# Kernel optimization log

Measured on AMD Instinct MI355X. Metric: run time of the kernel, lower is better.

## Reference

```python
import jax, jax.numpy as jnp
import numpy as np

N = 100000       # nodes
E = 1600000      # edges (before self-loops)
D_IN = 128       # input feature dim
HID = 16         # hidden channels per head
HEADS = 4
D_OUT = 32       # output communities
NEG_SLOPE = 0.2  # PyG GATConv default leaky_relu slope


def setup_inputs() -> dict:
    key = jax.random.key(0)
    ks = jax.random.split(key, 10)
    s = 0.1
    x = jax.random.normal(ks[0], (N, D_IN), jnp.float32)
    edge_index = jax.random.randint(ks[1], (2, E), 0, N, dtype=jnp.int64)
    W1 = jax.random.normal(ks[2], (D_IN, HEADS * HID), jnp.float32) * s
    a_src1 = jax.random.normal(ks[3], (HEADS, HID), jnp.float32) * s
    a_dst1 = jax.random.normal(ks[4], (HEADS, HID), jnp.float32) * s
    b1 = jnp.zeros((HEADS * HID,), jnp.float32)
    W2 = jax.random.normal(ks[5], (HEADS * HID, D_OUT), jnp.float32) * s
    a_src2 = jax.random.normal(ks[6], (1, D_OUT), jnp.float32) * s
    a_dst2 = jax.random.normal(ks[7], (1, D_OUT), jnp.float32) * s
    b2 = jnp.zeros((D_OUT,), jnp.float32)
    return {"x": x, "edge_index": edge_index, "W1": W1, "a_src1": a_src1,
            "a_dst1": a_dst1, "b1": b1, "W2": W2, "a_src2": a_src2,
            "a_dst2": a_dst2, "b2": b2}


def _segment_softmax(logits, seg, n):
    # softmax over edges grouped by destination node (per head)
    m = jax.ops.segment_max(logits, seg, num_segments=n)
    m = jnp.where(jnp.isfinite(m), m, 0.0)  # guard empty segments
    e = jnp.exp(logits - m[seg])
    z = jax.ops.segment_sum(e, seg, num_segments=n)
    return e / (z[seg] + 1e-16)


def _gat_conv(x, src, dst, W, a_src, a_dst, bias, heads, out_c, concat):
    n = x.shape[0]
    h = (x @ W).reshape(n, heads, out_c)                 # [N,H,C]
    al_s = jnp.einsum('nhc,hc->nh', h, a_src)            # [N,H]
    al_d = jnp.einsum('nhc,hc->nh', h, a_dst)            # [N,H]
    logits = jax.nn.leaky_relu(al_s[src] + al_d[dst], NEG_SLOPE)  # [E,H]
    alpha = _segment_softmax(logits, dst, n)             # [E,H]
    msg = h[src] * alpha[..., None]                      # [E,H,C]
    out = jax.ops.segment_sum(msg, dst, num_segments=n)  # [N,H,C]
    out = out.reshape(n, heads * out_c) if concat else out.mean(axis=1)
    return out + bias


def reference(x, edge_index, W1, a_src1, a_dst1, b1, W2, a_src2, a_dst2, b2):
    loops = jnp.arange(N, dtype=edge_index.dtype)
    src = jnp.concatenate([edge_index[0], loops])
    dst = jnp.concatenate([edge_index[1], loops])
    h = _gat_conv(x, src, dst, W1, a_src1, a_dst1, b1, HEADS, HID, True)
    h = jax.nn.elu(h)
    return _gat_conv(h, src, dst, W2, a_src2, a_dst2, b2, 1, D_OUT, False)
```

## Files before the change

kernel.cpp:

```cpp
#include <hip/hip_runtime.h>
#include <hip/hip_fp16.h>
#include <math.h>

#define NN 100000
#define EE 1600000
#define DIN 128
#define C1 64
#define C2 32
#define NEG 0.2f

#define NB 1024
#define BSH 7
#define EPB 4096
#define NGEMM 1563
#define NCHIST 391

static __device__ __forceinline__ float leaky(float x) { return fmaxf(x, NEG * x); }

__global__ __launch_bounds__(256, 2) void k_gemm1_chist(
    const float* __restrict__ x, const float* __restrict__ W1,
    const float* __restrict__ a_s, const float* __restrict__ a_d,
    __half* __restrict__ h1h, float* __restrict__ als, float* __restrict__ ald,
    const int* __restrict__ ei, int* __restrict__ bhist) {
    __shared__ float xs[64 * 128];
    __shared__ float wsh[128 * 64];
    int t = threadIdx.x;
    if (blockIdx.x >= NGEMM) {
        int* h = (int*)xs;
        for (int i = t; i < NB; i += 256) h[i] = 0;
        __syncthreads();
        const int4* d4p = (const int4*)(ei + EE);
        int i40 = (blockIdx.x - NGEMM) * (EPB / 4);
#pragma unroll
        for (int j = 0; j < 4; j++) {
            int idx = i40 + t + 256 * j;
            if (idx < EE / 4) {
                int4 d4 = d4p[idx];
                atomicAdd(&h[d4.x >> BSH], 1);
                atomicAdd(&h[d4.y >> BSH], 1);
                atomicAdd(&h[d4.z >> BSH], 1);
                atomicAdd(&h[d4.w >> BSH], 1);
            }
        }
        __syncthreads();
        for (int i = t; i < NB; i += 256) {
            int c = h[i];
            if (c) atomicAdd(&bhist[i], c);
        }
        return;
    }
    int base = blockIdx.x * 64;
    for (int i = t; i < 2048; i += 256) ((float4*)wsh)[i] = ((const float4*)W1)[i];
    int maxn = NN - base;
    if (maxn > 64) maxn = 64;
    for (int i = t; i < 2048; i += 256) {
        int flat = i * 4;
        int n = flat >> 7;
        if (n < maxn) *(float4*)&xs[flat] = *(const float4*)&x[(size_t)(base + n) * 128 + (flat & 127)];
    }
    __syncthreads();
    int w = t >> 6, c = t & 63;
    int nb = w * 16;
    float acc[16];
#pragma unroll
    for (int j = 0; j < 16; j++) acc[j] = 0.f;
    for (int k = 0; k < 128; k += 4) {
        float w0 = wsh[k * 64 + c], w1 = wsh[(k + 1) * 64 + c];
        float w2 = wsh[(k + 2) * 64 + c], w3 = wsh[(k + 3) * 64 + c];
#pragma unroll
        for (int j = 0; j < 16; j++) {
            float4 xv = *(float4*)&xs[(nb + j) * 128 + k];
            acc[j] = fmaf(xv.x, w0, acc[j]);
            acc[j] = fmaf(xv.y, w1, acc[j]);
            acc[j] = fmaf(xv.z, w2, acc[j]);
            acc[j] = fmaf(xv.w, w3, acc[j]);
        }
    }
    float s_a = a_s[c], d_a = a_d[c];
    int hd = c >> 4;
#pragma unroll
    for (int j = 0; j < 16; j++) {
        int n = base + nb + j;
        float v = acc[j];
        float vs = v * s_a, vd = v * d_a;
#pragma unroll
        for (int off = 1; off < 16; off <<= 1) {
            vs += __shfl_xor(vs, off, 64);
            vd += __shfl_xor(vd, off, 64);
        }
        if (n < NN) {
            h1h[(size_t)n * 64 + c] = __float2half(v);
            if ((c & 15) == 0) {
                als[n * 4 + hd] = vs;
                ald[n * 4 + hd] = vd;
            }
        }
    }
}


__global__ __launch_bounds__(256) void k_bscan(const int* __restrict__ bhist,
                                               int* __restrict__ gbase, int* __restrict__ gcur) {
    __shared__ int s[256];
    int t = threadIdx.x;
    int base = t * 4;
    int v[4];
    int run = 0;
#pragma unroll
    for (int j = 0; j < 4; j++) {
        v[j] = run;
        run += bhist[base + j];
    }
    int val = run;
    s[t] = val;
    __syncthreads();
    for (int off = 1; off < 256; off <<= 1) {
        int add = (t >= off) ? s[t - off] : 0;
        __syncthreads();
        val += add;
        s[t] = val;
        __syncthreads();
    }
    int texcl = val - run;
#pragma unroll
    for (int j = 0; j < 4; j++) {
        gbase[base + j] = texcl + v[j];
        gcur[base + j] = texcl + v[j];
    }
}

__global__ __launch_bounds__(256) void k_bin(const int* __restrict__ ei, int* __restrict__ gcur,
                                             int* __restrict__ binned) {
    __shared__ int h[NB];
    __shared__ int base[NB];
    int t = threadIdx.x;
    for (int i = t; i < NB; i += 256) h[i] = 0;
    __syncthreads();
    const int4* s4p = (const int4*)ei;
    const int4* d4p = (const int4*)(ei + EE);
    int i40 = blockIdx.x * (EPB / 4);
    int4 s4[4], d4[4];
    bool val[4];
#pragma unroll
    for (int j = 0; j < 4; j++) {
        int idx = i40 + t + 256 * j;
        val[j] = idx < EE / 4;
        if (val[j]) {
            s4[j] = s4p[idx];
            d4[j] = d4p[idx];
            atomicAdd(&h[d4[j].x >> BSH], 1);
            atomicAdd(&h[d4[j].y >> BSH], 1);
            atomicAdd(&h[d4[j].z >> BSH], 1);
            atomicAdd(&h[d4[j].w >> BSH], 1);
        }
    }
    __syncthreads();
    for (int i = t; i < NB; i += 256) {
        int c = h[i];
        if (c) base[i] = atomicAdd(&gcur[i], c);
        h[i] = 0;
    }
    __syncthreads();
#pragma unroll
    for (int j = 0; j < 4; j++) {
        if (val[j]) {
            int ss[4] = {s4[j].x, s4[j].y, s4[j].z, s4[j].w};
            int dd[4] = {d4[j].x, d4[j].y, d4[j].z, d4[j].w};
#pragma unroll
            for (int q = 0; q < 4; q++) {
                int b = dd[q] >> BSH;
                int r = atomicAdd(&h[b], 1);
                binned[base[b] + r] = (ss[q] << 7) | (dd[q] & 127);
            }
        }
    }
}

__global__ __launch_bounds__(256) void k_bsort(const int* __restrict__ binned,
                                               const int* __restrict__ gbase,
                                               const int* __restrict__ bhist,
                                               int* __restrict__ rs, int* __restrict__ deg,
                                               int* __restrict__ csr) {
    __shared__ int h[128], cur[128], sc[128];
    int b = blockIdx.x, t = threadIdx.x;
    if (t < 128) h[t] = 0;
    __syncthreads();
    int gb = gbase[b], cnt = bhist[b];
    for (int i = t; i < cnt; i += 256) atomicAdd(&h[binned[gb + i] & 127], 1);
    __syncthreads();
    if (t < 128) sc[t] = h[t];
    __syncthreads();
    for (int off = 1; off < 128; off <<= 1) {
        int add = 0;
        if (t < 128 && t >= off) add = sc[t - off];
        __syncthreads();
        if (t < 128) sc[t] += add;
        __syncthreads();
    }
    if (t < 128) {
        int node = b * 128 + t;
        int excl = sc[t] - h[t];
        if (node < NN) {
            rs[node] = gb + excl;
            deg[node] = h[t];
        }
        cur[t] = excl;
    }
    __syncthreads();
    for (int i = t; i < cnt; i += 256) {
        int e = binned[gb + i];
        int r = atomicAdd(&cur[e & 127], 1);
        csr[gb + r] = e >> 7;
    }
}

__global__ __launch_bounds__(256, 4) void k_edge1(
    const int* __restrict__ csr, const int* __restrict__ rs, const int* __restrict__ deg,
    const __half* __restrict__ h1h, const float* __restrict__ als, const float* __restrict__ ald,
    const float* __restrict__ b1, const float* __restrict__ W2,
    const float* __restrict__ as2, const float* __restrict__ ad2,
    __half* __restrict__ h2h, float* __restrict__ als2, float* __restrict__ ald2) {
    __shared__ float wsh[64 * 32];
    __shared__ float xld[4][64];
    __shared__ float2 epl[4][4][65];
    int t = threadIdx.x;
    for (int i = t; i < 512; i += 256) ((float4*)wsh)[i] = ((const float4*)W2)[i];
    int w = t >> 6, lane = t & 63;
    int n = blockIdx.x * 4 + w;
    float4 ad4 = *(const float4*)&ald[n * 4];
    float4 an4 = *(const float4*)&als[n * 4];
    float ls0 = leaky(an4.x + ad4.x), ls1 = leaky(an4.y + ad4.y);
    float ls2 = leaky(an4.z + ad4.z), ls3 = leaky(an4.w + ad4.w);
    const __half2* h1p = (const __half2*)h1h;
    int cc = lane & 31, eh = lane >> 5;
    int hd2 = cc >> 3;
    float z = 0.f, acc0 = 0.f, acc1 = 0.f;
    if (eh == 0) {
        float2 fs = __half22float2(h1p[n * 32 + cc]);
        z = 1.f;
        acc0 = fs.x;
        acc1 = fs.y;
    }
    int s0 = rs[n], d = deg[n];
    for (int i0 = 0; i0 < d; i0 += 64) {
        int e = i0 + lane;
        int src = 0;
        float4 a4 = make_float4(-1e30f, -1e30f, -1e30f, -1e30f);
        if (e < d) {
            src = csr[s0 + e];
            a4 = *(const float4*)&als[src * 4];
        }
        float fsrc = __int_as_float(src);
        epl[w][0][lane] = make_float2(fsrc, __expf(leaky(a4.x + ad4.x) - ls0));
        epl[w][1][lane] = make_float2(fsrc, __expf(leaky(a4.y + ad4.y) - ls1));
        epl[w][2][lane] = make_float2(fsrc, __expf(leaky(a4.z + ad4.z) - ls2));
        epl[w][3][lane] = make_float2(fsrc, __expf(leaky(a4.w + ad4.w) - ls3));
        int cnt = d - i0;
        if (cnt > 64) cnt = 64;
        int i = eh;
        for (; i + 14 < cnt; i += 16) {
            float2 q0 = epl[w][hd2][i], q1 = epl[w][hd2][i + 2];
            float2 q2 = epl[w][hd2][i + 4], q3 = epl[w][hd2][i + 6];
            float2 q4 = epl[w][hd2][i + 8], q5 = epl[w][hd2][i + 10];
            float2 q6 = epl[w][hd2][i + 12], q7 = epl[w][hd2][i + 14];
            float2 f0 = __half22float2(h1p[__float_as_int(q0.x) * 32 + cc]);
            float2 f1 = __half22float2(h1p[__float_as_int(q1.x) * 32 + cc]);
            float2 f2 = __half22float2(h1p[__float_as_int(q2.x) * 32 + cc]);
            float2 f3 = __half22float2(h1p[__float_as_int(q3.x) * 32 + cc]);
            float2 f4 = __half22float2(h1p[__float_as_int(q4.x) * 32 + cc]);
            float2 f5 = __half22float2(h1p[__float_as_int(q5.x) * 32 + cc]);
            float2 f6 = __half22float2(h1p[__float_as_int(q6.x) * 32 + cc]);
            float2 f7 = __half22float2(h1p[__float_as_int(q7.x) * 32 + cc]);
            z += ((q0.y + q1.y) + (q2.y + q3.y)) + ((q4.y + q5.y) + (q6.y + q7.y));
            acc0 = fmaf(q0.y, f0.x, acc0); acc1 = fmaf(q0.y, f0.y, acc1);
            acc0 = fmaf(q1.y, f1.x, acc0); acc1 = fmaf(q1.y, f1.y, acc1);
            acc0 = fmaf(q2.y, f2.x, acc0); acc1 = fmaf(q2.y, f2.y, acc1);
            acc0 = fmaf(q3.y, f3.x, acc0); acc1 = fmaf(q3.y, f3.y, acc1);
            acc0 = fmaf(q4.y, f4.x, acc0); acc1 = fmaf(q4.y, f4.y, acc1);
            acc0 = fmaf(q5.y, f5.x, acc0); acc1 = fmaf(q5.y, f5.y, acc1);
            acc0 = fmaf(q6.y, f6.x, acc0); acc1 = fmaf(q6.y, f6.y, acc1);
            acc0 = fmaf(q7.y, f7.x, acc0); acc1 = fmaf(q7.y, f7.y, acc1);
        }
        for (; i + 6 < cnt; i += 8) {
            float2 q0 = epl[w][hd2][i], q1 = epl[w][hd2][i + 2];
            float2 q2 = epl[w][hd2][i + 4], q3 = epl[w][hd2][i + 6];
            float2 f0 = __half22float2(h1p[__float_as_int(q0.x) * 32 + cc]);
            float2 f1 = __half22float2(h1p[__float_as_int(q1.x) * 32 + cc]);
            float2 f2 = __half22float2(h1p[__float_as_int(q2.x) * 32 + cc]);
            float2 f3 = __half22float2(h1p[__float_as_int(q3.x) * 32 + cc]);
            z += (q0.y + q1.y) + (q2.y + q3.y);
            acc0 = fmaf(q0.y, f0.x, acc0); acc1 = fmaf(q0.y, f0.y, acc1);
            acc0 = fmaf(q1.y, f1.x, acc0); acc1 = fmaf(q1.y, f1.y, acc1);
            acc0 = fmaf(q2.y, f2.x, acc0); acc1 = fmaf(q2.y, f2.y, acc1);
            acc0 = fmaf(q3.y, f3.x, acc0); acc1 = fmaf(q3.y, f3.y, acc1);
        }
        for (; i < cnt; i += 2) {
            float2 q = epl[w][hd2][i];
            float2 f = __half22float2(h1p[__float_as_int(q.x) * 32 + cc]);
            z += q.y;
            acc0 = fmaf(q.y, f.x, acc0);
            acc1 = fmaf(q.y, f.y, acc1);
        }
    }
    acc0 += __shfl_xor(acc0, 32, 64);
    acc1 += __shfl_xor(acc1, 32, 64);
    z += __shfl_xor(z, 32, 64);
    float zi = __frcp_rn(z + 1e-16f);
    float o0 = acc0 * zi + b1[2 * cc];
    float o1 = acc1 * zi + b1[2 * cc + 1];
    float xv0 = o0 > 0.f ? o0 : __expf(o0) - 1.f;
    float xv1 = o1 > 0.f ? o1 : __expf(o1) - 1.f;
    if (eh == 0) {
        xld[w][2 * cc] = xv0;
        xld[w][2 * cc + 1] = xv1;
    }
    __syncthreads();

    int hi = lane >> 5, c2 = lane & 31;
    float accn = 0.f;
#pragma unroll
    for (int k = 0; k < 32; k++) {
        float xk = xld[w][hi * 32 + k];
        accn = fmaf(xk, wsh[(hi * 32 + k) * 32 + c2], accn);
    }
    accn += __shfl_xor(accn, 32, 64);
    float vs = accn * as2[c2], vd = accn * ad2[c2];
#pragma unroll
    for (int off = 1; off < 32; off <<= 1) {
        vs += __shfl_xor(vs, off, 64);
        vd += __shfl_xor(vd, off, 64);
    }
    if (lane < 32) h2h[(size_t)n * 32 + lane] = __float2half(accn);
    if (lane == 0) {
        als2[n] = vs;
        ald2[n] = vd;
    }
}

__global__ __launch_bounds__(256, 4) void k_edge2(
    const int* __restrict__ csr, const int* __restrict__ rs, const int* __restrict__ deg,
    const __half* __restrict__ h2h, const float* __restrict__ als, const float* __restrict__ ald,
    const float* __restrict__ b2, float* __restrict__ out) {
    __shared__ float2 pst[4][64];
    int t = threadIdx.x;
    int w = t >> 6, lane = t & 63;
    int n = blockIdx.x * 4 + w;
    int cc = lane & 15, eq = lane >> 4;
    float ad = ald[n];
    float lself = leaky(als[n] + ad);
    const __half2* h2p = (const __half2*)h2h;
    float z = 0.f, acc0 = 0.f, acc1 = 0.f;
    if (eq == 0) {
        float2 fs = __half22float2(h2p[n * 16 + cc]);
        z = 1.f;
        acc0 = fs.x;
        acc1 = fs.y;
    }
    int s0 = rs[n], d = deg[n];
    for (int i0 = 0; i0 < d; i0 += 64) {
        int e = i0 + lane;
        int src = 0;
        float av = -1e30f;
        if (e < d) {
            src = csr[s0 + e];
            av = als[src];
        }
        float p = __expf(leaky(av + ad) - lself);
        pst[w][lane] = make_float2(__int_as_float(src), p);
        int cnt = d - i0;
        if (cnt > 64) cnt = 64;
        int i = eq;
        for (; i + 12 < cnt; i += 16) {
            float2 qA = pst[w][i], qB = pst[w][i + 4], qC = pst[w][i + 8], qD = pst[w][i + 12];
            int sA = __float_as_int(qA.x), sB = __float_as_int(qB.x);
            int sC = __float_as_int(qC.x), sD = __float_as_int(qD.x);
            float2 fA = __half22float2(h2p[sA * 16 + cc]);
            float2 fB = __half22float2(h2p[sB * 16 + cc]);
            float2 fC = __half22float2(h2p[sC * 16 + cc]);
            float2 fD = __half22float2(h2p[sD * 16 + cc]);
            z += (qA.y + qB.y) + (qC.y + qD.y);
            acc0 = fmaf(qA.y, fA.x, acc0); acc1 = fmaf(qA.y, fA.y, acc1);
            acc0 = fmaf(qB.y, fB.x, acc0); acc1 = fmaf(qB.y, fB.y, acc1);
            acc0 = fmaf(qC.y, fC.x, acc0); acc1 = fmaf(qC.y, fC.y, acc1);
            acc0 = fmaf(qD.y, fD.x, acc0); acc1 = fmaf(qD.y, fD.y, acc1);
        }
        for (; i < cnt; i += 4) {
            float2 q = pst[w][i];
            int sA = __float_as_int(q.x);
            float pA = q.y;
            float2 f = __half22float2(h2p[sA * 16 + cc]);
            z += pA;
            acc0 = fmaf(pA, f.x, acc0);
            acc1 = fmaf(pA, f.y, acc1);
        }
    }
    acc0 += __shfl_xor(acc0, 16, 64);
    acc0 += __shfl_xor(acc0, 32, 64);
    acc1 += __shfl_xor(acc1, 16, 64);
    acc1 += __shfl_xor(acc1, 32, 64);
    z += __shfl_xor(z, 16, 64);
    z += __shfl_xor(z, 32, 64);
    if (eq == 0) {
        float zi = __frcp_rn(z + 1e-16f);
        float o0 = acc0 * zi + b2[2 * cc];
        float o1 = acc1 * zi + b2[2 * cc + 1];
        *(float2*)&out[(size_t)n * 32 + 2 * cc] = make_float2(o0, o1);
    }
}

extern "C" void kernel_launch(void* const* d_in, const int* in_sizes, int n_in,
                              void* d_out, int out_size, void* d_ws, size_t ws_size,
                              hipStream_t stream) {
    const float* x = (const float*)d_in[0];
    const int* ei = (const int*)d_in[1];
    const float* W1 = (const float*)d_in[2];
    const float* as1 = (const float*)d_in[3];
    const float* ad1 = (const float*)d_in[4];
    const float* b1 = (const float*)d_in[5];
    const float* W2 = (const float*)d_in[6];
    const float* as2 = (const float*)d_in[7];
    const float* ad2 = (const float*)d_in[8];
    const float* b2 = (const float*)d_in[9];
    float* out = (float*)d_out;

    char* p = (char*)d_ws;
    auto alloc = [&](size_t bytes) -> char* {
        char* r = p;
        p += (bytes + 255) & ~(size_t)255;
        return r;
    };
    int* csr = (int*)alloc((size_t)EE * 4);
    int* rs = (int*)alloc((size_t)NN * 4);
    int* deg = (int*)alloc((size_t)NN * 4);
    int* bhist = (int*)alloc(NB * 4);
    int* gbase = (int*)alloc(NB * 4);
    int* gcur = (int*)alloc(NB * 4);
    __half* h1h = (__half*)alloc((size_t)NN * C1 * 2);
    float* als1 = (float*)alloc((size_t)NN * 4 * 4);
    float* ald1 = (float*)alloc((size_t)NN * 4 * 4);
    char* regionX = alloc((size_t)NN * C2 * 2 + (size_t)NN * 8 + 512);
    int* binned = (int*)regionX;
    __half* h2h = (__half*)regionX;
    float* als2 = (float*)(regionX + (size_t)NN * C2 * 2);
    float* ald2 = (float*)(regionX + (size_t)NN * C2 * 2 + (size_t)NN * 4);
    (void)ws_size;

    hipMemsetAsync(bhist, 0, NB * 4, stream);

    k_gemm1_chist<<<NGEMM + NCHIST, 256, 0, stream>>>(x, W1, as1, ad1, h1h, als1, ald1,
                                                      ei, bhist);
    k_bscan<<<1, 256, 0, stream>>>(bhist, gbase, gcur);
    k_bin<<<NCHIST, 256, 0, stream>>>(ei, gcur, binned);
    k_bsort<<<(NN + 127) / 128, 256, 0, stream>>>(binned, gbase, bhist, rs, deg, csr);

    k_edge1<<<NN / 4, 256, 0, stream>>>(csr, rs, deg, h1h, als1, ald1, b1, W2, as2, ad2,
                                        h2h, als2, ald2);
    k_edge2<<<NN / 4, 256, 0, stream>>>(csr, rs, deg, h2h, als2, ald2, b2, out);
}
```

Measured before the change: 332.3 us.

## Map more nodes per wavefront in edge kernels and pack row start with degree

k_edge1 now assigns one node per half-wavefront (32 lanes) instead of one per wavefront, and k_edge2 one node per quarter-wavefront (16 lanes). This removes the cross-lane reductions and the idle lanes that low-degree nodes (average degree 16) left in the old edge-split scheme. Source indices are pre-shifted into byte offsets to simplify gather addressing. The row start and degree arrays are merged into one int2 array. W2 is stored transposed in shared memory so the second GEMM can use float4 reads, and the grids shrink to match. Nodes with large degree now run more serial iterations per group, which risks more load imbalance within a wavefront.

Result: faster. 293.0 us (-11.8%).

```diff
diff --git a/kernel.cpp b/kernel.cpp
--- a/kernel.cpp
+++ b/kernel.cpp
@@ -179,7 +179,7 @@
 __global__ __launch_bounds__(256) void k_bsort(const int* __restrict__ binned,
                                                const int* __restrict__ gbase,
                                                const int* __restrict__ bhist,
-                                               int* __restrict__ rs, int* __restrict__ deg,
+                                               int2* __restrict__ rsdeg,
                                                int* __restrict__ csr) {
     __shared__ int h[128], cur[128], sc[128];
     int b = blockIdx.x, t = threadIdx.x;
@@ -200,10 +200,7 @@
     if (t < 128) {
         int node = b * 128 + t;
         int excl = sc[t] - h[t];
-        if (node < NN) {
-            rs[node] = gb + excl;
-            deg[node] = h[t];
-        }
+        if (node < NN) rsdeg[node] = make_int2(gb + excl, h[t]);
         cur[t] = excl;
     }
     __syncthreads();
@@ -215,62 +212,58 @@
 }
 
 __global__ __launch_bounds__(256, 4) void k_edge1(
-    const int* __restrict__ csr, const int* __restrict__ rs, const int* __restrict__ deg,
+    const int* __restrict__ csr, const int2* __restrict__ rsdeg,
     const __half* __restrict__ h1h, const float* __restrict__ als, const float* __restrict__ ald,
     const float* __restrict__ b1, const float* __restrict__ W2,
     const float* __restrict__ as2, const float* __restrict__ ad2,
     __half* __restrict__ h2h, float* __restrict__ als2, float* __restrict__ ald2) {
-    __shared__ float wsh[64 * 32];
-    __shared__ float xld[4][64];
-    __shared__ float2 epl[4][4][65];
+    __shared__ float wsh[32][68];
+    __shared__ float xld[4][2][64];
+    __shared__ float2 epl[4][2][4][33];
     int t = threadIdx.x;
-    for (int i = t; i < 512; i += 256) ((float4*)wsh)[i] = ((const float4*)W2)[i];
-    int w = t >> 6, lane = t & 63;
-    int n = blockIdx.x * 4 + w;
+    for (int i = t; i < 2048; i += 256) wsh[i & 31][i >> 5] = W2[i];
+    int w = t >> 6, lane = t & 63, half = lane >> 5, ln = lane & 31;
+    int n = blockIdx.x * 8 + w * 2 + half;
     float4 ad4 = *(const float4*)&ald[n * 4];
     float4 an4 = *(const float4*)&als[n * 4];
     float ls0 = leaky(an4.x + ad4.x), ls1 = leaky(an4.y + ad4.y);
     float ls2 = leaky(an4.z + ad4.z), ls3 = leaky(an4.w + ad4.w);
     const __half2* h1p = (const __half2*)h1h;
-    int cc = lane & 31, eh = lane >> 5;
-    int hd2 = cc >> 3;
-    float z = 0.f, acc0 = 0.f, acc1 = 0.f;
-    if (eh == 0) {
-        float2 fs = __half22float2(h1p[n * 32 + cc]);
-        z = 1.f;
-        acc0 = fs.x;
-        acc1 = fs.y;
-    }
-    int s0 = rs[n], d = deg[n];
-    for (int i0 = 0; i0 < d; i0 += 64) {
-        int e = i0 + lane;
+    const char* h1c = (const char*)h1h;
+    int hd2 = ln >> 3;
+    int coff = ln * 4;
+    float2 fs = __half22float2(h1p[n * 32 + ln]);
+    float z = 1.f, acc0 = fs.x, acc1 = fs.y;
+    int2 rd = rsdeg[n];
+    int s0 = rd.x, d = rd.y;
+    for (int i0 = 0; i0 < d; i0 += 32) {
+        int e = i0 + ln;
         int src = 0;
         float4 a4 = make_float4(-1e30f, -1e30f, -1e30f, -1e30f);
         if (e < d) {
             src = csr[s0 + e];
             a4 = *(const float4*)&als[src * 4];
         }
-        float fsrc = __int_as_float(src);
-        epl[w][0][lane] = make_float2(fsrc, __expf(leaky(a4.x + ad4.x) - ls0));
-        epl[w][1][lane] = make_float2(fsrc, __expf(leaky(a4.y + ad4.y) - ls1));
-        epl[w][2][lane] = make_float2(fsrc, __expf(leaky(a4.z + ad4.z) - ls2));
-        epl[w][3][lane] = make_float2(fsrc, __expf(leaky(a4.w + ad4.w) - ls3));
+        float fsb = __int_as_float(src << 7);
+        epl[w][half][0][ln] = make_float2(fsb, __expf(leaky(a4.x + ad4.x) - ls0));
+        epl[w][half][1][ln] = make_float2(fsb, __expf(leaky(a4.y + ad4.y) - ls1));
+        epl[w][half][2][ln] = make_float2(fsb, __expf(leaky(a4.z + ad4.z) - ls2));
+        epl[w][half][3][ln] = make_float2(fsb, __expf(leaky(a4.w + ad4.w) - ls3));
         int cnt = d - i0;
-        if (cnt > 64) cnt = 64;
-        int i = eh;
-        for (; i + 14 < cnt; i += 16) {
-            float2 q0 = epl[w][hd2][i], q1 = epl[w][hd2][i + 2];
-            float2 q2 = epl[w][hd2][i + 4], q3 = epl[w][hd2][i + 6];
-            float2 q4 = epl[w][hd2][i + 8], q5 = epl[w][hd2][i + 10];
-            float2 q6 = epl[w][hd2][i + 12], q7 = epl[w][hd2][i + 14];
-            float2 f0 = __half22float2(h1p[__float_as_int(q0.x) * 32 + cc]);
-            float2 f1 = __half22float2(h1p[__float_as_int(q1.x) * 32 + cc]);
-            float2 f2 = __half22float2(h1p[__float_as_int(q2.x) * 32 + cc]);
-            float2 f3 = __half22float2(h1p[__float_as_int(q3.x) * 32 + cc]);
-            float2 f4 = __half22float2(h1p[__float_as_int(q4.x) * 32 + cc]);
-            float2 f5 = __half22float2(h1p[__float_as_int(q5.x) * 32 + cc]);
-            float2 f6 = __half22float2(h1p[__float_as_int(q6.x) * 32 + cc]);
-            float2 f7 = __half22float2(h1p[__float_as_int(q7.x) * 32 + cc]);
+        if (cnt > 32) cnt = 32;
+        const float2* ep = epl[w][half][hd2];
+        int i = 0;
+        for (; i + 7 < cnt; i += 8) {
+            float2 q0 = ep[i], q1 = ep[i + 1], q2 = ep[i + 2], q3 = ep[i + 3];
+            float2 q4 = ep[i + 4], q5 = ep[i + 5], q6 = ep[i + 6], q7 = ep[i + 7];
+            float2 f0 = __half22float2(*(const __half2*)(h1c + __float_as_int(q0.x) + coff));
+            float2 f1 = __half22float2(*(const __half2*)(h1c + __float_as_int(q1.x) + coff));
+            float2 f2 = __half22float2(*(const __half2*)(h1c + __float_as_int(q2.x) + coff));
+            float2 f3 = __half22float2(*(const __half2*)(h1c + __float_as_int(q3.x) + coff));
+            float2 f4 = __half22float2(*(const __half2*)(h1c + __float_as_int(q4.x) + coff));
+            float2 f5 = __half22float2(*(const __half2*)(h1c + __float_as_int(q5.x) + coff));
+            float2 f6 = __half22float2(*(const __half2*)(h1c + __float_as_int(q6.x) + coff));
+            float2 f7 = __half22float2(*(const __half2*)(h1c + __float_as_int(q7.x) + coff));
             z += ((q0.y + q1.y) + (q2.y + q3.y)) + ((q4.y + q5.y) + (q6.y + q7.y));
             acc0 = fmaf(q0.y, f0.x, acc0); acc1 = fmaf(q0.y, f0.y, acc1);
             acc0 = fmaf(q1.y, f1.x, acc0); acc1 = fmaf(q1.y, f1.y, acc1);
@@ -281,131 +274,113 @@
             acc0 = fmaf(q6.y, f6.x, acc0); acc1 = fmaf(q6.y, f6.y, acc1);
             acc0 = fmaf(q7.y, f7.x, acc0); acc1 = fmaf(q7.y, f7.y, acc1);
         }
-        for (; i + 6 < cnt; i += 8) {
-            float2 q0 = epl[w][hd2][i], q1 = epl[w][hd2][i + 2];
-            float2 q2 = epl[w][hd2][i + 4], q3 = epl[w][hd2][i + 6];
-            float2 f0 = __half22float2(h1p[__float_as_int(q0.x) * 32 + cc]);
-            float2 f1 = __half22float2(h1p[__float_as_int(q1.x) * 32 + cc]);
-            float2 f2 = __half22float2(h1p[__float_as_int(q2.x) * 32 + cc]);
-            float2 f3 = __half22float2(h1p[__float_as_int(q3.x) * 32 + cc]);
+        for (; i + 3 < cnt; i += 4) {
+            float2 q0 = ep[i], q1 = ep[i + 1], q2 = ep[i + 2], q3 = ep[i + 3];
+            float2 f0 = __half22float2(*(const __half2*)(h1c + __float_as_int(q0.x) + coff));
+            float2 f1 = __half22float2(*(const __half2*)(h1c + __float_as_int(q1.x) + coff));
+            float2 f2 = __half22float2(*(const __half2*)(h1c + __float_as_int(q2.x) + coff));
+            float2 f3 = __half22float2(*(const __half2*)(h1c + __float_as_int(q3.x) + coff));
             z += (q0.y + q1.y) + (q2.y + q3.y);
             acc0 = fmaf(q0.y, f0.x, acc0); acc1 = fmaf(q0.y, f0.y, acc1);
             acc0 = fmaf(q1.y, f1.x, acc0); acc1 = fmaf(q1.y, f1.y, acc1);
             acc0 = fmaf(q2.y, f2.x, acc0); acc1 = fmaf(q2.y, f2.y, acc1);
             acc0 = fmaf(q3.y, f3.x, acc0); acc1 = fmaf(q3.y, f3.y, acc1);
         }
-        for (; i < cnt; i += 2) {
-            float2 q = epl[w][hd2][i];
-            float2 f = __half22float2(h1p[__float_as_int(q.x) * 32 + cc]);
+        for (; i < cnt; i++) {
+            float2 q = ep[i];
+            float2 f = __half22float2(*(const __half2*)(h1c + __float_as_int(q.x) + coff));
             z += q.y;
             acc0 = fmaf(q.y, f.x, acc0);
             acc1 = fmaf(q.y, f.y, acc1);
         }
     }
-    acc0 += __shfl_xor(acc0, 32, 64);
-    acc1 += __shfl_xor(acc1, 32, 64);
-    z += __shfl_xor(z, 32, 64);
     float zi = __frcp_rn(z + 1e-16f);
-    float o0 = acc0 * zi + b1[2 * cc];
-    float o1 = acc1 * zi + b1[2 * cc + 1];
+    float o0 = acc0 * zi + b1[2 * ln];
+    float o1 = acc1 * zi + b1[2 * ln + 1];
     float xv0 = o0 > 0.f ? o0 : __expf(o0) - 1.f;
     float xv1 = o1 > 0.f ? o1 : __expf(o1) - 1.f;
-    if (eh == 0) {
-        xld[w][2 * cc] = xv0;
-        xld[w][2 * cc + 1] = xv1;
-    }
-    __syncthreads();
-
-    int hi = lane >> 5, c2 = lane & 31;
+    xld[w][half][2 * ln] = xv0;
+    xld[w][half][2 * ln + 1] = xv1;
+    __syncthreads();
+
     float accn = 0.f;
 #pragma unroll
-    for (int k = 0; k < 32; k++) {
-        float xk = xld[w][hi * 32 + k];
-        accn = fmaf(xk, wsh[(hi * 32 + k) * 32 + c2], accn);
-    }
-    accn += __shfl_xor(accn, 32, 64);
-    float vs = accn * as2[c2], vd = accn * ad2[c2];
+    for (int k4 = 0; k4 < 16; k4++) {
+        float4 xk = *(float4*)&xld[w][half][k4 * 4];
+        float4 wk = *(float4*)&wsh[ln][k4 * 4];
+        accn = fmaf(xk.x, wk.x, accn);
+        accn = fmaf(xk.y, wk.y, accn);
+        accn = fmaf(xk.z, wk.z, accn);
+        accn = fmaf(xk.w, wk.w, accn);
+    }
+    h2h[(size_t)n * 32 + ln] = __float2half(accn);
+    float vs = accn * as2[ln], vd = accn * ad2[ln];
 #pragma unroll
     for (int off = 1; off < 32; off <<= 1) {
         vs += __shfl_xor(vs, off, 64);
         vd += __shfl_xor(vd, off, 64);
     }
-    if (lane < 32) h2h[(size_t)n * 32 + lane] = __float2half(accn);
-    if (lane == 0) {
+    if (ln == 0) {
         als2[n] = vs;
         ald2[n] = vd;
     }
 }
 
 __global__ __launch_bounds__(256, 4) void k_edge2(
-    const int* __restrict__ csr, const int* __restrict__ rs, const int* __restrict__ deg,
+    const int* __restrict__ csr, const int2* __restrict__ rsdeg,
     const __half* __restrict__ h2h, const float* __restrict__ als, const float* __restrict__ ald,
     const float* __restrict__ b2, float* __restrict__ out) {
-    __shared__ float2 pst[4][64];
+    __shared__ float2 pst[4][4][17];
     int t = threadIdx.x;
-    int w = t >> 6, lane = t & 63;
-    int n = blockIdx.x * 4 + w;
-    int cc = lane & 15, eq = lane >> 4;
+    int w = t >> 6, lane = t & 63, q = lane >> 4, ln = lane & 15;
+    int n = blockIdx.x * 16 + w * 4 + q;
     float ad = ald[n];
     float lself = leaky(als[n] + ad);
     const __half2* h2p = (const __half2*)h2h;
-    float z = 0.f, acc0 = 0.f, acc1 = 0.f;
-    if (eq == 0) {
-        float2 fs = __half22float2(h2p[n * 16 + cc]);
-        z = 1.f;
-        acc0 = fs.x;
-        acc1 = fs.y;
-    }
-    int s0 = rs[n], d = deg[n];
-    for (int i0 = 0; i0 < d; i0 += 64) {
-        int e = i0 + lane;
+    const char* h2c = (const char*)h2h;
+    int coff = ln * 4;
+    float2 fs = __half22float2(h2p[n * 16 + ln]);
+    float z = 1.f, acc0 = fs.x, acc1 = fs.y;
+    int2 rd = rsdeg[n];
+    int s0 = rd.x, d = rd.y;
+    for (int i0 = 0; i0 < d; i0 += 16) {
+        int e = i0 + ln;
         int src = 0;
         float av = -1e30f;
         if (e < d) {
             src = csr[s0 + e];
             av = als[src];
         }
-        float p = __expf(leaky(av + ad) - lself);
-        pst[w][lane] = make_float2(__int_as_float(src), p);
+        pst[w][q][ln] = make_float2(__int_as_float(src << 6),
+                                    __expf(leaky(av + ad) - lself));
         int cnt = d - i0;
-        if (cnt > 64) cnt = 64;
-        int i = eq;
-        for (; i + 12 < cnt; i += 16) {
-            float2 qA = pst[w][i], qB = pst[w][i + 4], qC = pst[w][i + 8], qD = pst[w][i + 12];
-            int sA = __float_as_int(qA.x), sB = __float_as_int(qB.x);
-            int sC = __float_as_int(qC.x), sD = __float_as_int(qD.x);
-            float2 fA = __half22float2(h2p[sA * 16 + cc]);
-            float2 fB = __half22float2(h2p[sB * 16 + cc]);
-            float2 fC = __half22float2(h2p[sC * 16 + cc]);
-            float2 fD = __half22float2(h2p[sD * 16 + cc]);
-            z += (qA.y + qB.y) + (qC.y + qD.y);
-            acc0 = fmaf(qA.y, fA.x, acc0); acc1 = fmaf(qA.y, fA.y, acc1);
-            acc0 = fmaf(qB.y, fB.x, acc0); acc1 = fmaf(qB.y, fB.y, acc1);
-            acc0 = fmaf(qC.y, fC.x, acc0); acc1 = fmaf(qC.y, fC.y, acc1);
-            acc0 = fmaf(qD.y, fD.x, acc0); acc1 = fmaf(qD.y, fD.y, acc1);
-        }
-        for (; i < cnt; i += 4) {
-            float2 q = pst[w][i];
-            int sA = __float_as_int(q.x);
-            float pA = q.y;
-            float2 f = __half22float2(h2p[sA * 16 + cc]);
-            z += pA;
-            acc0 = fmaf(pA, f.x, acc0);
-            acc1 = fmaf(pA, f.y, acc1);
-        }
-    }
-    acc0 += __shfl_xor(acc0, 16, 64);
-    acc0 += __shfl_xor(acc0, 32, 64);
-    acc1 += __shfl_xor(acc1, 16, 64);
-    acc1 += __shfl_xor(acc1, 32, 64);
-    z += __shfl_xor(z, 16, 64);
-    z += __shfl_xor(z, 32, 64);
-    if (eq == 0) {
-        float zi = __frcp_rn(z + 1e-16f);
-        float o0 = acc0 * zi + b2[2 * cc];
-        float o1 = acc1 * zi + b2[2 * cc + 1];
-        *(float2*)&out[(size_t)n * 32 + 2 * cc] = make_float2(o0, o1);
-    }
+        if (cnt > 16) cnt = 16;
+        const float2* ep = pst[w][q];
+        int i = 0;
+        for (; i + 3 < cnt; i += 4) {
+            float2 q0 = ep[i], q1 = ep[i + 1], q2 = ep[i + 2], q3 = ep[i + 3];
+            float2 f0 = __half22float2(*(const __half2*)(h2c + __float_as_int(q0.x) + coff));
+            float2 f1 = __half22float2(*(const __half2*)(h2c + __float_as_int(q1.x) + coff));
+            float2 f2 = __half22float2(*(const __half2*)(h2c + __float_as_int(q2.x) + coff));
+            float2 f3 = __half22float2(*(const __half2*)(h2c + __float_as_int(q3.x) + coff));
+            z += (q0.y + q1.y) + (q2.y + q3.y);
+            acc0 = fmaf(q0.y, f0.x, acc0); acc1 = fmaf(q0.y, f0.y, acc1);
+            acc0 = fmaf(q1.y, f1.x, acc0); acc1 = fmaf(q1.y, f1.y, acc1);
+            acc0 = fmaf(q2.y, f2.x, acc0); acc1 = fmaf(q2.y, f2.y, acc1);
+            acc0 = fmaf(q3.y, f3.x, acc0); acc1 = fmaf(q3.y, f3.y, acc1);
+        }
+        for (; i < cnt; i++) {
+            float2 qq = ep[i];
+            float2 f = __half22float2(*(const __half2*)(h2c + __float_as_int(qq.x) + coff));
+            z += qq.y;
+            acc0 = fmaf(qq.y, f.x, acc0);
+            acc1 = fmaf(qq.y, f.y, acc1);
+        }
+    }
+    float zi = __frcp_rn(z + 1e-16f);
+    float o0 = acc0 * zi + b2[2 * ln];
+    float o1 = acc1 * zi + b2[2 * ln + 1];
+    *(float2*)&out[(size_t)n * 32 + 2 * ln] = make_float2(o0, o1);
 }
 
 extern "C" void kernel_launch(void* const* d_in, const int* in_sizes, int n_in,
@@ -430,8 +405,7 @@
         return r;
     };
     int* csr = (int*)alloc((size_t)EE * 4);
-    int* rs = (int*)alloc((size_t)NN * 4);
-    int* deg = (int*)alloc((size_t)NN * 4);
+    int2* rsdeg = (int2*)alloc((size_t)NN * 8);
     int* bhist = (int*)alloc(NB * 4);
     int* gbase = (int*)alloc(NB * 4);
     int* gcur = (int*)alloc(NB * 4);
@@ -451,9 +425,9 @@
                                                       ei, bhist);
     k_bscan<<<1, 256, 0, stream>>>(bhist, gbase, gcur);
     k_bin<<<NCHIST, 256, 0, stream>>>(ei, gcur, binned);
-    k_bsort<<<(NN + 127) / 128, 256, 0, stream>>>(binned, gbase, bhist, rs, deg, csr);
-
-    k_edge1<<<NN / 4, 256, 0, stream>>>(csr, rs, deg, h1h, als1, ald1, b1, W2, as2, ad2,
+    k_bsort<<<(NN + 127) / 128, 256, 0, stream>>>(binned, gbase, bhist, rsdeg, csr);
+
+    k_edge1<<<NN / 8, 256, 0, stream>>>(csr, rsdeg, h1h, als1, ald1, b1, W2, as2, ad2,
                                         h2h, als2, ald2);
-    k_edge2<<<NN / 4, 256, 0, stream>>>(csr, rs, deg, h2h, als2, ald2, b2, out);
-}
+    k_edge2<<<NN / 16, 256, 0, stream>>>(csr, rsdeg, h2h, als2, ald2, b2, out);
+}
```
